# Optimization experiments

Hardware: AMD Instinct MI355X
Metric: run time of the kernel (lower is better)

Reference implementation:

```python
import jax, jax.numpy as jnp
import numpy as np

N_NODES = 50000
N_EDGES = 800000
D = 128
HEADS = 4
HEAD_DIM = D // HEADS
N_LAYERS = 3
NEG_SLOPE = 0.2


def setup_inputs() -> dict:
    key = jax.random.key(0)
    ks = jax.random.split(key, 10)
    x = jax.random.normal(ks[0], (N_NODES, D), dtype=jnp.float32)
    edge_index = jax.random.randint(ks[1], (2, N_EDGES), 0, N_NODES, dtype=jnp.int32)
    s = 1.0 / np.sqrt(D)
    gcn_w = jax.random.normal(ks[2], (N_LAYERS, D, D), dtype=jnp.float32) * s
    gcn_b = jnp.zeros((N_LAYERS, D), dtype=jnp.float32)
    gat_w = jax.random.normal(ks[3], (N_LAYERS, D, D), dtype=jnp.float32) * s
    gat_att_src = jax.random.normal(ks[4], (N_LAYERS, HEADS, HEAD_DIM), dtype=jnp.float32) * s
    gat_att_dst = jax.random.normal(ks[5], (N_LAYERS, HEADS, HEAD_DIM), dtype=jnp.float32) * s
    gat_b = jnp.zeros((N_LAYERS, D), dtype=jnp.float32)
    ln_g = jnp.ones((N_LAYERS, D), dtype=jnp.float32)
    ln_b = jnp.zeros((N_LAYERS, D), dtype=jnp.float32)
    return {"x": x, "edge_index": edge_index, "gcn_w": gcn_w, "gcn_b": gcn_b,
            "gat_w": gat_w, "gat_att_src": gat_att_src, "gat_att_dst": gat_att_dst,
            "gat_b": gat_b, "ln_g": ln_g, "ln_b": ln_b}


def _gcn(x, src, dst, n, w, b):
    # PyG GCNConv: self-loops (already in src/dst), symmetric normalization
    xw = x @ w                                             # [N, D]
    deg = jax.ops.segment_sum(jnp.ones_like(dst, dtype=xw.dtype), dst, num_segments=n)
    dinv = jax.lax.rsqrt(deg)                              # deg >= 1 due to self-loops
    norm = dinv[src] * dinv[dst]                           # [E]
    out = jax.ops.segment_sum(xw[src] * norm[:, None], dst, num_segments=n)
    return out + b


def _gat(x, src, dst, n, w, att_src, att_dst, b):
    # PyG GATConv, concat heads, self-loops already in src/dst
    xw = (x @ w).reshape(n, HEADS, HEAD_DIM)               # [N, H, Dh]
    a_src = (xw * att_src).sum(-1)                         # [N, H]
    a_dst = (xw * att_dst).sum(-1)                         # [N, H]
    e = jax.nn.leaky_relu(a_src[src] + a_dst[dst], NEG_SLOPE)  # [E, H]
    m = jax.ops.segment_max(e, dst, num_segments=n)        # [N, H]
    ee = jnp.exp(e - m[dst])
    z = jax.ops.segment_sum(ee, dst, num_segments=n)       # [N, H]
    alpha = ee / z[dst]                                    # [E, H]
    out = jax.ops.segment_sum(xw[src] * alpha[:, :, None], dst, num_segments=n)
    return out.reshape(n, HEADS * HEAD_DIM) + b


def _layernorm(x, g, b, eps=1e-5):
    mu = x.mean(-1, keepdims=True)
    var = ((x - mu) ** 2).mean(-1, keepdims=True)
    return (x - mu) * jax.lax.rsqrt(var + eps) * g + b


def reference(x, edge_index, gcn_w, gcn_b, gat_w, gat_att_src, gat_att_dst, gat_b, ln_g, ln_b):
    n = x.shape[0]
    loops = jnp.arange(n, dtype=edge_index.dtype)
    src = jnp.concatenate([edge_index[0], loops])
    dst = jnp.concatenate([edge_index[1], loops])
    h = x
    for i in range(N_LAYERS):
        h_gcn = _gcn(h, src, dst, n, gcn_w[i], gcn_b[i])
        h_att = _gat(h_gcn, src, dst, n, gat_w[i], gat_att_src[i], gat_att_dst[i], gat_b[i])
        h = _layernorm(h_att + h_gcn, ln_g[i], ln_b[i])
        h = jax.nn.relu(h)  # dropout is identity in eval mode
    return h
```

## Files before the change

### kernel.cpp

```cpp
#include <hip/hip_runtime.h>

#define NN 50000
#define NE 800000
#define NOUT (NN * 128)
#define PF_TOTAL 100608

typedef unsigned int u32;
typedef unsigned short u16;

typedef __attribute__((ext_vector_type(4))) float f32x4;
typedef __attribute__((ext_vector_type(8))) short bf16x8;

__device__ __forceinline__ float bf2f(u16 u) { return __uint_as_float(((u32)u) << 16); }
__device__ __forceinline__ u32 f2bf_u(float f) {
  u32 u = __float_as_uint(f);
  u += 0x7FFFu + ((u >> 16) & 1u);
  return u >> 16;
}
__device__ __forceinline__ u32 pk2(float a, float b) {
  return f2bf_u(a) | (f2bf_u(b) << 16);
}
__device__ __forceinline__ float lo_f(u32 v) { return __uint_as_float(v << 16); }
__device__ __forceinline__ float hi_f(u32 v) { return __uint_as_float(v & 0xFFFF0000u); }
__device__ __forceinline__ float h2f(u16 h) {
  u32 sg = ((u32)h >> 15) & 1u, e = ((u32)h >> 10) & 0x1Fu, mm = (u32)h & 0x3FFu;
  u32 o;
  if (e == 0u) o = sg << 31;
  else if (e == 31u) o = (sg << 31) | 0x7F800000u | (mm << 13);
  else o = (sg << 31) | ((e + 112u) << 23) | (mm << 13);
  return __uint_as_float(o);
}
__device__ __forceinline__ float lrelu(float x) { return x > 0.f ? x : 0.2f * x; }
__device__ __forceinline__ u32 umin32(u32 a, u32 b) { return a < b ? a : b; }

__device__ __forceinline__ float cvt_one(const void* p, int j, u32 fmode) {
  if (fmode == 1u) return ((const float*)p)[j];
  if (fmode == 2u) return h2f(((const u16*)p)[j]);
  return bf2f(((const u16*)p)[j]);
}

__global__ __launch_bounds__(256) void MultiScaleGNN_54769422958784_kernel(
    float* out, float val, int n) {
  int i = blockIdx.x * 256 + threadIdx.x;
  if (i < n) out[i] = val;
}

__global__ __launch_bounds__(64) void detect_kernel(const u32* lng, const int* ei,
                                                    u32* flag) {
  if (threadIdx.x == 0) {
    u32 v0 = lng[0], v1 = lng[1];
    u32 fm;
    if (v0 == 0x3F803F80u && v1 == 0x3F803F80u) fm = 0u;
    else if (v0 == 0x3F800000u && v1 == 0x3F800000u) fm = 1u;
    else if (v0 == 0x3C003C00u && v1 == 0x3C003C00u) fm = 2u;
    else fm = 1u;
    flag[0] = fm;
    flag[1] = ((ei[1] | ei[3] | ei[5] | ei[7]) == 0) ? 1u : 0u;
  }
}

__global__ __launch_bounds__(256) void cvt_x_kernel(const void* in, u32* outh, int n64,
                                                    const u32* flag) {
  u32 fm = flag[0];
  int i = blockIdx.x * 256 + threadIdx.x;
  if (i >= n64) return;
  int node = i >> 6, w = i & 63;
  float a = cvt_one(in, node * 128 + w * 2, fm);
  float b = cvt_one(in, node * 128 + w * 2 + 1, fm);
  outh[i] = pk2(a, b);
}

__global__ __launch_bounds__(256) void cvt_params_kernel(const void* g0, const void* g1,
                                                         const void* g2, const void* g3,
                                                         const void* g4, const void* g5,
                                                         const void* g6, const void* g7,
                                                         float* out, const u32* flag) {
  u32 fm = flag[0];
  int i = blockIdx.x * 256 + threadIdx.x;
  if (i >= PF_TOTAL) return;
  int offs[9] = {0, 49152, 49536, 98688, 99072, 99456, 99840, 100224, 100608};
  const void* ptrs[8] = {g0, g1, g2, g3, g4, g5, g6, g7};
  int r = 0;
  while (i >= offs[r + 1]) r++;
  out[i] = cvt_one(ptrs[r], i - offs[r], fm);
}

__global__ __launch_bounds__(256) void cvt_wt_kernel(const float* __restrict__ pf,
                                                     u32* __restrict__ wt) {
  int i = blockIdx.x * 256 + threadIdx.x;
  if (i >= 49152) return;
  int mat = i >> 13;
  int rem = i & 8191;
  int kk = rem >> 7;
  int n = rem & 127;
  const float* W = pf + (mat < 3 ? (size_t)mat * 16384 : 49536 + (size_t)(mat - 3) * 16384);
  float a = W[(2 * kk) * 128 + n];
  float b = W[(2 * kk + 1) * 128 + n];
  wt[(size_t)mat * 8192 + n * 64 + kk] = pk2(a, b);
}

__global__ __launch_bounds__(256) void zero1_kernel(u32* a, int n) {
  int i = blockIdx.x * 256 + threadIdx.x;
  if (i < n) a[i] = 0u;
}

__global__ __launch_bounds__(256) void rank_kernel(const int* ei, u32* cnt, u32* rank,
                                                   int e, int n, const u32* flag) {
  int i = blockIdx.x * blockDim.x + threadIdx.x;
  if (i >= e) return;
  int d = flag[1] ? ei[2 * e + 2 * i] : ei[e + i];
  u32 r = 0u;
  if ((u32)d < (u32)n) r = atomicAdd(&cnt[d], 1u);
  rank[i] = r;
}

__device__ __forceinline__ u32 wave_incl_scan(u32 v, int lane) {
#pragma unroll
  for (int off = 1; off < 64; off <<= 1) {
    u32 t = (u32)__shfl_up((int)v, off);
    if (lane >= off) v += t;
  }
  return v;
}

__global__ __launch_bounds__(256) void scan_sum_kernel(const u32* counts, u32* bsums,
                                                       int n) {
  __shared__ u32 ws[4];
  int i = blockIdx.x * 256 + threadIdx.x;
  int lane = threadIdx.x & 63, wid = threadIdx.x >> 6;
  u32 c = (i < n) ? counts[i] : 0u;
#pragma unroll
  for (int off = 32; off; off >>= 1) c += (u32)__shfl_xor((int)c, off);
  if (lane == 0) ws[wid] = c;
  __syncthreads();
  if (threadIdx.x == 0) bsums[blockIdx.x] = ws[0] + ws[1] + ws[2] + ws[3];
}

__global__ __launch_bounds__(256) void scan_bsums_kernel(u32* bsums, u32* rowptr, int nb,
                                                         int n) {
  __shared__ u32 ws[4];
  int tid = threadIdx.x, lane = tid & 63, wid = tid >> 6;
  u32 v = (tid < nb) ? bsums[tid] : 0u;
  u32 incl = wave_incl_scan(v, lane);
  if (lane == 63) ws[wid] = incl;
  __syncthreads();
  u32 wo = 0u;
  for (int w = 0; w < wid; w++) wo += ws[w];
  u32 excl = incl - v + wo;
  if (tid < nb) bsums[tid] = excl;
  if (tid == 0) rowptr[n] = ws[0] + ws[1] + ws[2] + ws[3];
}

__global__ __launch_bounds__(256) void scan_write_kernel(const u32* counts,
                                                         const u32* bsums, u32* rowptr,
                                                         float* dinv, int n) {
  __shared__ u32 ws[4];
  int b = blockIdx.x;
  int i = b * 256 + threadIdx.x;
  int lane = threadIdx.x & 63, wid = threadIdx.x >> 6;
  u32 c = (i < n) ? counts[i] : 0u;
  u32 incl = wave_incl_scan(c, lane);
  if (lane == 63) ws[wid] = incl;
  __syncthreads();
  u32 wo = bsums[b];
  for (int w = 0; w < wid; w++) wo += ws[w];
  u32 excl = incl - c + wo;
  if (i < n) {
    rowptr[i] = excl;
    dinv[i] = rsqrtf((float)(c + 1u));
  }
}

__global__ __launch_bounds__(256) void place_kernel(const int* ei, const u32* rowptr,
                                                    const u32* rank, int* col, int e,
                                                    int n, const u32* flag) {
  int i = blockIdx.x * blockDim.x + threadIdx.x;
  if (i >= e) return;
  u32 em = flag[1];
  int s = em ? ei[2 * i] : ei[i];
  int d = em ? ei[2 * e + 2 * i] : ei[e + i];
  if ((u32)d >= (u32)n) return;
  u32 p = rowptr[d] + rank[i];
  if (p < (u32)e) col[p] = ((u32)s < (u32)n) ? s : 0;
}

__global__ __launch_bounds__(256) void gemm_mfma_kernel(
    const u32* __restrict__ Ah, const u32* __restrict__ WTh, u32* __restrict__ Oh,
    const float* __restrict__ dinv, const float* __restrict__ att_s,
    const float* __restrict__ att_d, float* __restrict__ asrc,
    float* __restrict__ adst, int M) {
  int tid = threadIdx.x;
  int wave = tid >> 6, lane = tid & 63;
  int p = lane & 15, g = lane >> 4;
  int r0 = blockIdx.x * 128 + wave * 32;
  int ra = r0 + p, rb = r0 + 16 + p;
  int rac = min(ra, M - 1), rbc = min(rb, M - 1);

  const u32* apA = Ah + (size_t)rac * 64 + g * 4;
  const u32* apB = Ah + (size_t)rbc * 64 + g * 4;
  uint4 bA[4], bB[4];
#pragma unroll
  for (int k0 = 0; k0 < 4; k0++) {
    bA[k0] = *(const uint4*)(apA + k0 * 16);
    bB[k0] = *(const uint4*)(apB + k0 * 16);
  }

  f32x4 acc0[8], acc1[8];
#pragma unroll
  for (int t = 0; t < 8; t++) {
    acc0[t] = (f32x4)0.f;
    acc1[t] = (f32x4)0.f;
  }

  const u32* wp = WTh + p * 64 + g * 4;
#pragma unroll
  for (int k0 = 0; k0 < 4; k0++) {
    bf16x8 fa = __builtin_bit_cast(bf16x8, bA[k0]);
    bf16x8 fb = __builtin_bit_cast(bf16x8, bB[k0]);
#pragma unroll
    for (int t = 0; t < 8; t++) {
      uint4 af = *(const uint4*)(wp + t * 1024 + k0 * 16);
      bf16x8 aw = __builtin_bit_cast(bf16x8, af);
      acc0[t] = __builtin_amdgcn_mfma_f32_16x16x32_bf16(aw, fa, acc0[t], 0, 0, 0);
      acc1[t] = __builtin_amdgcn_mfma_f32_16x16x32_bf16(aw, fb, acc1[t], 0, 0, 0);
    }
  }

#pragma unroll
  for (int i = 0; i < 2; i++) {
    int r = r0 + i * 16 + p;
    if (r < M) {
      float sc = dinv ? dinv[r] : 1.0f;
      u32* orow = Oh + (size_t)r * 64;
      float hs[4] = {0.f, 0.f, 0.f, 0.f};
      float hd[4] = {0.f, 0.f, 0.f, 0.f};
#pragma unroll
      for (int t = 0; t < 8; t++) {
        f32x4 v = (i == 0) ? acc0[t] : acc1[t];
        float v0 = v[0] * sc, v1 = v[1] * sc, v2 = v[2] * sc, v3 = v[3] * sc;
        *(uint2*)(orow + t * 8 + g * 2) = make_uint2(pk2(v0, v1), pk2(v2, v3));
        if (att_s) {
          float4 wsv = *(const float4*)(att_s + t * 16 + g * 4);
          float4 wdv = *(const float4*)(att_d + t * 16 + g * 4);
          int h = t >> 1;
          hs[h] += v0 * wsv.x + v1 * wsv.y + v2 * wsv.z + v3 * wsv.w;
          hd[h] += v0 * wdv.x + v1 * wdv.y + v2 * wdv.z + v3 * wdv.w;
        }
      }
      if (att_s) {
#pragma unroll
        for (int h = 0; h < 4; h++) {
          hs[h] += __shfl_xor(hs[h], 16);
          hs[h] += __shfl_xor(hs[h], 32);
          hd[h] += __shfl_xor(hd[h], 16);
          hd[h] += __shfl_xor(hd[h], 32);
        }
        if (g == 0) {
          *(float4*)(asrc + (size_t)r * 4) = make_float4(hs[0], hs[1], hs[2], hs[3]);
          *(float4*)(adst + (size_t)r * 4) = make_float4(hd[0], hd[1], hd[2], hd[3]);
        }
      }
    }
  }
}

__global__ __launch_bounds__(256) void gcn_agg_kernel(const u32* __restrict__ xh,
                                                      const int* col, const u32* rowptr,
                                                      const float* dinv, const float* bias,
                                                      u32* __restrict__ outh, int n) {
  __shared__ int lds_s[8][32];
  int g = threadIdx.x >> 5;
  int l = threadIdx.x & 31;
  int d = blockIdx.x * 8 + g;
  if (d >= n) return;
  u32 start = umin32(rowptr[d], (u32)NE), end = umin32(rowptr[d + 1], (u32)NE);
  float4 acc = make_float4(0.f, 0.f, 0.f, 0.f);
  for (u32 base = start; base < end; base += 32) {
    u32 i = base + l;
    int cnt = (int)umin32(32u, end - base);
    if (i < end) lds_s[g][l] = col[i];
#pragma unroll 4
    for (int j = 0; j < cnt; j++) {
      int s = lds_s[g][j];
      uint2 v = *(const uint2*)(xh + (size_t)s * 64 + l * 2);
      acc.x += lo_f(v.x);
      acc.y += hi_f(v.x);
      acc.z += lo_f(v.y);
      acc.w += hi_f(v.y);
    }
  }
  int c0 = l * 4;
  uint2 sv = *(const uint2*)(xh + (size_t)d * 64 + l * 2);
  float dd = dinv[d];
  float o0 = dd * (acc.x + lo_f(sv.x)) + bias[c0];
  float o1 = dd * (acc.y + hi_f(sv.x)) + bias[c0 + 1];
  float o2 = dd * (acc.z + lo_f(sv.y)) + bias[c0 + 2];
  float o3 = dd * (acc.w + hi_f(sv.y)) + bias[c0 + 3];
  *(uint2*)(outh + (size_t)d * 64 + l * 2) = make_uint2(pk2(o0, o1), pk2(o2, o3));
}

__global__ __launch_bounds__(256) void gat_agg_kernel(
    const u32* __restrict__ xh, const float* a_src4, const float* a_dst4, const int* col,
    const u32* rowptr, const u32* __restrict__ hgcnh, const float* gat_b,
    const float* ln_g, const float* ln_b, u32* __restrict__ outh,
    float* __restrict__ outf, int n) {
  __shared__ u32 lds_s[8][32];
  __shared__ float lds_ee[8][32][4];
  int g = threadIdx.x >> 5;
  int l = threadIdx.x & 31;
  int head4 = l >> 3;
  int d = blockIdx.x * 8 + g;
  if (d >= n) return;
  u32 start = umin32(rowptr[d], (u32)NE), end = umin32(rowptr[d + 1], (u32)NE);
  float4 ad = *(const float4*)(a_dst4 + (size_t)d * 4);
  float4 asl = *(const float4*)(a_src4 + (size_t)d * 4);
  float4 es;
  es.x = lrelu(asl.x + ad.x);
  es.y = lrelu(asl.y + ad.y);
  es.z = lrelu(asl.z + ad.z);
  es.w = lrelu(asl.w + ad.w);
  float4 m = es;
  float4 zp = make_float4(0.f, 0.f, 0.f, 0.f);
  float4 acc = make_float4(0.f, 0.f, 0.f, 0.f);
  for (u32 base = start; base < end; base += 32) {
    u32 i = base + l;
    int cnt = (int)umin32(32u, end - base);
    bool act = i < end;
    float4 lg = make_float4(-1e30f, -1e30f, -1e30f, -1e30f);
    int s = 0;
    if (act) {
      s = col[i];
      float4 a = *(const float4*)(a_src4 + (size_t)s * 4);
      lg.x = lrelu(a.x + ad.x);
      lg.y = lrelu(a.y + ad.y);
      lg.z = lrelu(a.z + ad.z);
      lg.w = lrelu(a.w + ad.w);
    }
    float4 cm = lg;
#pragma unroll
    for (int off = 16; off; off >>= 1) {
      cm.x = fmaxf(cm.x, __shfl_xor(cm.x, off));
      cm.y = fmaxf(cm.y, __shfl_xor(cm.y, off));
      cm.z = fmaxf(cm.z, __shfl_xor(cm.z, off));
      cm.w = fmaxf(cm.w, __shfl_xor(cm.w, off));
    }
    float4 mn;
    mn.x = fmaxf(m.x, cm.x);
    mn.y = fmaxf(m.y, cm.y);
    mn.z = fmaxf(m.z, cm.z);
    mn.w = fmaxf(m.w, cm.w);
    float4 f;
    f.x = __expf(m.x - mn.x);
    f.y = __expf(m.y - mn.y);
    f.z = __expf(m.z - mn.z);
    f.w = __expf(m.w - mn.w);
    m = mn;
    zp.x *= f.x;
    zp.y *= f.y;
    zp.z *= f.z;
    zp.w *= f.w;
    float fsel = (head4 == 0) ? f.x : (head4 == 1) ? f.y : (head4 == 2) ? f.z : f.w;
    acc.x *= fsel;
    acc.y *= fsel;
    acc.z *= fsel;
    acc.w *= fsel;
    if (act) {
      float ex = __expf(lg.x - m.x);
      float ey = __expf(lg.y - m.y);
      float ez = __expf(lg.z - m.z);
      float ew = __expf(lg.w - m.w);
      zp.x += ex;
      zp.y += ey;
      zp.z += ez;
      zp.w += ew;
      lds_s[g][l] = (u32)s;
      *(float4*)&lds_ee[g][l][0] = make_float4(ex, ey, ez, ew);
    }
#pragma unroll 4
    for (int j = 0; j < cnt; j++) {
      u32 sg = lds_s[g][j];
      float w = lds_ee[g][j][head4];
      uint2 v = *(const uint2*)(xh + (size_t)sg * 64 + l * 2);
      acc.x = fmaf(w, lo_f(v.x), acc.x);
      acc.y = fmaf(w, hi_f(v.x), acc.y);
      acc.z = fmaf(w, lo_f(v.y), acc.z);
      acc.w = fmaf(w, hi_f(v.y), acc.w);
    }
  }
  float4 ees;
  ees.x = __expf(es.x - m.x);
  ees.y = __expf(es.y - m.y);
  ees.z = __expf(es.z - m.z);
  ees.w = __expf(es.w - m.w);
#pragma unroll
  for (int off = 16; off; off >>= 1) {
    zp.x += __shfl_xor(zp.x, off);
    zp.y += __shfl_xor(zp.y, off);
    zp.z += __shfl_xor(zp.z, off);
    zp.w += __shfl_xor(zp.w, off);
  }
  zp.x += ees.x;
  zp.y += ees.y;
  zp.z += ees.z;
  zp.w += ees.w;
  float wsel = (head4 == 0) ? ees.x : (head4 == 1) ? ees.y : (head4 == 2) ? ees.z : ees.w;
  float zsel = (head4 == 0) ? zp.x : (head4 == 1) ? zp.y : (head4 == 2) ? zp.z : zp.w;
  int c0 = l * 4;
  uint2 sv = *(const uint2*)(xh + (size_t)d * 64 + l * 2);
  acc.x = fmaf(wsel, lo_f(sv.x), acc.x);
  acc.y = fmaf(wsel, hi_f(sv.x), acc.y);
  acc.z = fmaf(wsel, lo_f(sv.y), acc.z);
  acc.w = fmaf(wsel, hi_f(sv.y), acc.w);
  float rz = 1.0f / zsel;
  uint2 hgv = *(const uint2*)(hgcnh + (size_t)d * 64 + l * 2);
  float t0 = acc.x * rz + gat_b[c0] + lo_f(hgv.x);
  float t1 = acc.y * rz + gat_b[c0 + 1] + hi_f(hgv.x);
  float t2 = acc.z * rz + gat_b[c0 + 2] + lo_f(hgv.y);
  float t3 = acc.w * rz + gat_b[c0 + 3] + hi_f(hgv.y);
  float ssum = t0 + t1 + t2 + t3;
#pragma unroll
  for (int off = 16; off; off >>= 1) ssum += __shfl_xor(ssum, off);
  float mu = ssum * (1.0f / 128.0f);
  float d0 = t0 - mu, d1 = t1 - mu, d2 = t2 - mu, d3 = t3 - mu;
  float vv = d0 * d0 + d1 * d1 + d2 * d2 + d3 * d3;
#pragma unroll
  for (int off = 16; off; off >>= 1) vv += __shfl_xor(vv, off);
  float rstd = rsqrtf(vv * (1.0f / 128.0f) + 1e-5f);
  float o0 = fmaxf(fmaf(d0 * rstd, ln_g[c0], ln_b[c0]), 0.f);
  float o1 = fmaxf(fmaf(d1 * rstd, ln_g[c0 + 1], ln_b[c0 + 1]), 0.f);
  float o2 = fmaxf(fmaf(d2 * rstd, ln_g[c0 + 2], ln_b[c0 + 2]), 0.f);
  float o3 = fmaxf(fmaf(d3 * rstd, ln_g[c0 + 3], ln_b[c0 + 3]), 0.f);
  if (outf) {
    *(float4*)(outf + (size_t)d * 128 + c0) = make_float4(o0, o1, o2, o3);
  } else {
    *(uint2*)(outh + (size_t)d * 64 + l * 2) = make_uint2(pk2(o0, o1), pk2(o2, o3));
  }
}

extern "C" void kernel_launch(void* const* d_in, const int* in_sizes, int n_in,
                              void* d_out, int out_size, void* d_ws, size_t ws_size,
                              hipStream_t stream) {
  const int N = NN, E = NE;
  (void)in_sizes;
  (void)n_in;
  (void)out_size;
  (void)ws_size;

  char* ws = (char*)d_ws;
  size_t off = 0;
  u32* xwh = (u32*)(ws + off);      off += (size_t)N * 64 * 4;
  u32* hbufh = (u32*)(ws + off);    off += (size_t)N * 64 * 4;
  u32* hgcnh = (u32*)(ws + off);    off += (size_t)N * 64 * 4;
  float* asrc = (float*)(ws + off); off += (size_t)N * 4 * 4;
  float* adst = (float*)(ws + off); off += (size_t)N * 4 * 4;
  float* dinv = (float*)(ws + off); off += (size_t)N * 4;
  u32* counts = (u32*)(ws + off);   off += (size_t)N * 4;
  u32* rowptr = (u32*)(ws + off);   off += (size_t)(N + 1) * 4 + 252;
  u32* rank = (u32*)(ws + off);     off += (size_t)E * 4;
  int* col = (int*)(ws + off);      off += (size_t)E * 4;
  float* pf = (float*)(ws + off);   off += (size_t)PF_TOTAL * 4;
  u32* wt = (u32*)(ws + off);       off += (size_t)49152 * 4;
  u32* bsums = (u32*)(ws + off);    off += 256 * 4;
  u32* flag = (u32*)(ws + off);     off += 256;

  const int* edge_index = (const int*)d_in[1];
  detect_kernel<<<1, 64, 0, stream>>>((const u32*)d_in[8], edge_index, flag);
  cvt_params_kernel<<<(PF_TOTAL + 255) / 256, 256, 0, stream>>>(
      d_in[2], d_in[3], d_in[4], d_in[5], d_in[6], d_in[7], d_in[8], d_in[9], pf, flag);
  cvt_wt_kernel<<<(49152 + 255) / 256, 256, 0, stream>>>(pf, wt);
  cvt_x_kernel<<<(N * 64 + 255) / 256, 256, 0, stream>>>(d_in[0], hbufh, N * 64, flag);
  zero1_kernel<<<(N + 255) / 256, 256, 0, stream>>>(counts, N);
  rank_kernel<<<(E + 255) / 256, 256, 0, stream>>>(edge_index, counts, rank, E, N, flag);
  {
    int nb = (N + 255) / 256;
    scan_sum_kernel<<<nb, 256, 0, stream>>>(counts, bsums, N);
    scan_bsums_kernel<<<1, 256, 0, stream>>>(bsums, rowptr, nb, N);
    scan_write_kernel<<<nb, 256, 0, stream>>>(counts, bsums, rowptr, dinv, N);
  }
  place_kernel<<<(E + 255) / 256, 256, 0, stream>>>(edge_index, rowptr, rank, col, E, N,
                                                    flag);

  const float* att_s = pf + 98688;
  const float* att_d = pf + 99072;
  const float* gcn_b = pf + 49152;
  const float* gat_b = pf + 99456;
  const float* ln_g = pf + 99840;
  const float* ln_b = pf + 100224;

  int gblocks = (N + 127) / 128;
  int ablocks = (N + 7) / 8;
  for (int l = 0; l < 3; l++) {
    gemm_mfma_kernel<<<gblocks, 256, 0, stream>>>(
        hbufh, wt + (size_t)l * 8192, xwh, dinv, (const float*)0, (const float*)0,
        (float*)0, (float*)0, N);
    gcn_agg_kernel<<<ablocks, 256, 0, stream>>>(xwh, col, rowptr, dinv, gcn_b + l * 128,
                                                hgcnh, N);
    gemm_mfma_kernel<<<gblocks, 256, 0, stream>>>(
        hgcnh, wt + (size_t)(3 + l) * 8192, xwh, (const float*)0, att_s + l * 128,
        att_d + l * 128, asrc, adst, N);
    gat_agg_kernel<<<ablocks, 256, 0, stream>>>(
        xwh, asrc, adst, col, rowptr, hgcnh, gat_b + l * 128, ln_g + l * 128,
        ln_b + l * 128, hbufh, (l < 2) ? (float*)0 : (float*)d_out, N);
  }
}
```

Before: 476.3 us.

## Bucket CSR neighbours by source-index chunk to improve gather locality

Edges are counted and placed per (destination, source-chunk) bucket, using eight chunks over the node range. Within each destination row the neighbour list is therefore roughly grouped by source index, so the gathers in the aggregation kernels touch more nearby memory. The scan is widened to cover eight times as many counters, and degree normalisation moves into a separate kernel that reads the bucketed rowptr. Preprocessing gets more work, and any locality gain is small because the average degree is only about 16 per row.

```diff
diff --git a/kernel.cpp b/kernel.cpp
--- a/kernel.cpp
+++ b/kernel.cpp
@@ -4,6 +4,9 @@
 #define NE 800000
 #define NOUT (NN * 128)
 #define PF_TOTAL 100608
+#define NCHUNK 8
+#define CHUNKSZ 6250
+#define NC4 (NN * NCHUNK)
 
 typedef unsigned int u32;
 typedef unsigned short u16;
@@ -108,9 +111,12 @@
                                                    int e, int n, const u32* flag) {
   int i = blockIdx.x * blockDim.x + threadIdx.x;
   if (i >= e) return;
-  int d = flag[1] ? ei[2 * e + 2 * i] : ei[e + i];
+  u32 em = flag[1];
+  int s = em ? ei[2 * i] : ei[i];
+  int d = em ? ei[2 * e + 2 * i] : ei[e + i];
+  int sp = ((u32)s < (u32)n) ? s : 0;
   u32 r = 0u;
-  if ((u32)d < (u32)n) r = atomicAdd(&cnt[d], 1u);
+  if ((u32)d < (u32)n) r = atomicAdd(&cnt[d * NCHUNK + sp / CHUNKSZ], 1u);
   rank[i] = r;
 }
 
@@ -126,19 +132,21 @@
 __global__ __launch_bounds__(256) void scan_sum_kernel(const u32* counts, u32* bsums,
                                                        int n) {
   __shared__ u32 ws[4];
-  int i = blockIdx.x * 256 + threadIdx.x;
-  int lane = threadIdx.x & 63, wid = threadIdx.x >> 6;
-  u32 c = (i < n) ? counts[i] : 0u;
-#pragma unroll
-  for (int off = 32; off; off >>= 1) c += (u32)__shfl_xor((int)c, off);
-  if (lane == 0) ws[wid] = c;
+  int tid = threadIdx.x, lane = tid & 63, wid = tid >> 6;
+  int i0 = blockIdx.x * 1024 + tid * 4;
+  u32 t = 0u;
+#pragma unroll
+  for (int k = 0; k < 4; k++) t += (i0 + k < n) ? counts[i0 + k] : 0u;
+#pragma unroll
+  for (int off = 32; off; off >>= 1) t += (u32)__shfl_xor((int)t, off);
+  if (lane == 0) ws[wid] = t;
   __syncthreads();
-  if (threadIdx.x == 0) bsums[blockIdx.x] = ws[0] + ws[1] + ws[2] + ws[3];
-}
-
-__global__ __launch_bounds__(256) void scan_bsums_kernel(u32* bsums, u32* rowptr, int nb,
+  if (tid == 0) bsums[blockIdx.x] = ws[0] + ws[1] + ws[2] + ws[3];
+}
+
+__global__ __launch_bounds__(512) void scan_bsums_kernel(u32* bsums, u32* rowptr, int nb,
                                                          int n) {
-  __shared__ u32 ws[4];
+  __shared__ u32 ws[8];
   int tid = threadIdx.x, lane = tid & 63, wid = tid >> 6;
   u32 v = (tid < nb) ? bsums[tid] : 0u;
   u32 incl = wave_incl_scan(v, lane);
@@ -148,30 +156,49 @@
   for (int w = 0; w < wid; w++) wo += ws[w];
   u32 excl = incl - v + wo;
   if (tid < nb) bsums[tid] = excl;
-  if (tid == 0) rowptr[n] = ws[0] + ws[1] + ws[2] + ws[3];
+  if (tid == 0) {
+    u32 tot = 0u;
+    for (int w = 0; w < 8; w++) tot += ws[w];
+    rowptr[n] = tot;
+  }
 }
 
 __global__ __launch_bounds__(256) void scan_write_kernel(const u32* counts,
                                                          const u32* bsums, u32* rowptr,
-                                                         float* dinv, int n) {
+                                                         int n) {
   __shared__ u32 ws[4];
+  int tid = threadIdx.x, lane = tid & 63, wid = tid >> 6;
   int b = blockIdx.x;
-  int i = b * 256 + threadIdx.x;
-  int lane = threadIdx.x & 63, wid = threadIdx.x >> 6;
-  u32 c = (i < n) ? counts[i] : 0u;
-  u32 incl = wave_incl_scan(c, lane);
+  int i0 = b * 1024 + tid * 4;
+  u32 c0 = (i0 + 0 < n) ? counts[i0 + 0] : 0u;
+  u32 c1 = (i0 + 1 < n) ? counts[i0 + 1] : 0u;
+  u32 c2 = (i0 + 2 < n) ? counts[i0 + 2] : 0u;
+  u32 c3 = (i0 + 3 < n) ? counts[i0 + 3] : 0u;
+  u32 ts = c0 + c1 + c2 + c3;
+  u32 incl = wave_incl_scan(ts, lane);
   if (lane == 63) ws[wid] = incl;
   __syncthreads();
   u32 wo = bsums[b];
   for (int w = 0; w < wid; w++) wo += ws[w];
-  u32 excl = incl - c + wo;
-  if (i < n) {
-    rowptr[i] = excl;
-    dinv[i] = rsqrtf((float)(c + 1u));
-  }
-}
-
-__global__ __launch_bounds__(256) void place_kernel(const int* ei, const u32* rowptr,
+  u32 excl = incl - ts + wo;
+  if (i0 + 0 < n) rowptr[i0 + 0] = excl;
+  excl += c0;
+  if (i0 + 1 < n) rowptr[i0 + 1] = excl;
+  excl += c1;
+  if (i0 + 2 < n) rowptr[i0 + 2] = excl;
+  excl += c2;
+  if (i0 + 3 < n) rowptr[i0 + 3] = excl;
+}
+
+__global__ __launch_bounds__(256) void dinv_kernel(const u32* __restrict__ rowptr4,
+                                                   float* __restrict__ dinv, int nn) {
+  int i = blockIdx.x * 256 + threadIdx.x;
+  if (i < nn)
+    dinv[i] = rsqrtf((float)(rowptr4[(size_t)i * NCHUNK + NCHUNK] -
+                             rowptr4[(size_t)i * NCHUNK] + 1u));
+}
+
+__global__ __launch_bounds__(256) void place_kernel(const int* ei, const u32* rowptr4,
                                                     const u32* rank, int* col, int e,
                                                     int n, const u32* flag) {
   int i = blockIdx.x * blockDim.x + threadIdx.x;
@@ -180,8 +207,9 @@
   int s = em ? ei[2 * i] : ei[i];
   int d = em ? ei[2 * e + 2 * i] : ei[e + i];
   if ((u32)d >= (u32)n) return;
-  u32 p = rowptr[d] + rank[i];
-  if (p < (u32)e) col[p] = ((u32)s < (u32)n) ? s : 0;
+  int sp = ((u32)s < (u32)n) ? s : 0;
+  u32 p = rowptr4[(size_t)d * NCHUNK + sp / CHUNKSZ] + rank[i];
+  if (p < (u32)e) col[p] = sp;
 }
 
 __global__ __launch_bounds__(256) void gemm_mfma_kernel(
@@ -265,7 +293,7 @@
 }
 
 __global__ __launch_bounds__(256) void gcn_agg_kernel(const u32* __restrict__ xh,
-                                                      const int* col, const u32* rowptr,
+                                                      const int* col, const u32* rowptr4,
                                                       const float* dinv, const float* bias,
                                                       u32* __restrict__ outh, int n) {
   __shared__ int lds_s[8][32];
@@ -273,7 +301,8 @@
   int l = threadIdx.x & 31;
   int d = blockIdx.x * 8 + g;
   if (d >= n) return;
-  u32 start = umin32(rowptr[d], (u32)NE), end = umin32(rowptr[d + 1], (u32)NE);
+  u32 start = umin32(rowptr4[(size_t)d * NCHUNK], (u32)NE);
+  u32 end = umin32(rowptr4[(size_t)d * NCHUNK + NCHUNK], (u32)NE);
   float4 acc = make_float4(0.f, 0.f, 0.f, 0.f);
   for (u32 base = start; base < end; base += 32) {
     u32 i = base + l;
@@ -301,7 +330,7 @@
 
 __global__ __launch_bounds__(256) void gat_agg_kernel(
     const u32* __restrict__ xh, const float* a_src4, const float* a_dst4, const int* col,
-    const u32* rowptr, const u32* __restrict__ hgcnh, const float* gat_b,
+    const u32* rowptr4, const u32* __restrict__ hgcnh, const float* gat_b,
     const float* ln_g, const float* ln_b, u32* __restrict__ outh,
     float* __restrict__ outf, int n) {
   __shared__ u32 lds_s[8][32];
@@ -311,7 +340,8 @@
   int head4 = l >> 3;
   int d = blockIdx.x * 8 + g;
   if (d >= n) return;
-  u32 start = umin32(rowptr[d], (u32)NE), end = umin32(rowptr[d + 1], (u32)NE);
+  u32 start = umin32(rowptr4[(size_t)d * NCHUNK], (u32)NE);
+  u32 end = umin32(rowptr4[(size_t)d * NCHUNK + NCHUNK], (u32)NE);
   float4 ad = *(const float4*)(a_dst4 + (size_t)d * 4);
   float4 asl = *(const float4*)(a_src4 + (size_t)d * 4);
   float4 es;
@@ -454,13 +484,13 @@
   float* asrc = (float*)(ws + off); off += (size_t)N * 4 * 4;
   float* adst = (float*)(ws + off); off += (size_t)N * 4 * 4;
   float* dinv = (float*)(ws + off); off += (size_t)N * 4;
-  u32* counts = (u32*)(ws + off);   off += (size_t)N * 4;
-  u32* rowptr = (u32*)(ws + off);   off += (size_t)(N + 1) * 4 + 252;
+  u32* counts4 = (u32*)(ws + off);  off += (size_t)NC4 * 4;
+  u32* rowptr4 = (u32*)(ws + off);  off += (size_t)(NC4 + 1) * 4 + 252;
   u32* rank = (u32*)(ws + off);     off += (size_t)E * 4;
   int* col = (int*)(ws + off);      off += (size_t)E * 4;
   float* pf = (float*)(ws + off);   off += (size_t)PF_TOTAL * 4;
   u32* wt = (u32*)(ws + off);       off += (size_t)49152 * 4;
-  u32* bsums = (u32*)(ws + off);    off += 256 * 4;
+  u32* bsums = (u32*)(ws + off);    off += 512 * 4;
   u32* flag = (u32*)(ws + off);     off += 256;
 
   const int* edge_index = (const int*)d_in[1];
@@ -469,15 +499,16 @@
       d_in[2], d_in[3], d_in[4], d_in[5], d_in[6], d_in[7], d_in[8], d_in[9], pf, flag);
   cvt_wt_kernel<<<(49152 + 255) / 256, 256, 0, stream>>>(pf, wt);
   cvt_x_kernel<<<(N * 64 + 255) / 256, 256, 0, stream>>>(d_in[0], hbufh, N * 64, flag);
-  zero1_kernel<<<(N + 255) / 256, 256, 0, stream>>>(counts, N);
-  rank_kernel<<<(E + 255) / 256, 256, 0, stream>>>(edge_index, counts, rank, E, N, flag);
+  zero1_kernel<<<(NC4 + 255) / 256, 256, 0, stream>>>(counts4, NC4);
+  rank_kernel<<<(E + 255) / 256, 256, 0, stream>>>(edge_index, counts4, rank, E, N, flag);
   {
-    int nb = (N + 255) / 256;
-    scan_sum_kernel<<<nb, 256, 0, stream>>>(counts, bsums, N);
-    scan_bsums_kernel<<<1, 256, 0, stream>>>(bsums, rowptr, nb, N);
-    scan_write_kernel<<<nb, 256, 0, stream>>>(counts, bsums, rowptr, dinv, N);
-  }
-  place_kernel<<<(E + 255) / 256, 256, 0, stream>>>(edge_index, rowptr, rank, col, E, N,
+    int nb = (NC4 + 1023) / 1024;
+    scan_sum_kernel<<<nb, 256, 0, stream>>>(counts4, bsums, NC4);
+    scan_bsums_kernel<<<1, 512, 0, stream>>>(bsums, rowptr4, nb, NC4);
+    scan_write_kernel<<<nb, 256, 0, stream>>>(counts4, bsums, rowptr4, NC4);
+  }
+  dinv_kernel<<<(N + 255) / 256, 256, 0, stream>>>(rowptr4, dinv, N);
+  place_kernel<<<(E + 255) / 256, 256, 0, stream>>>(edge_index, rowptr4, rank, col, E, N,
                                                     flag);
 
   const float* att_s = pf + 98688;
@@ -493,13 +524,13 @@
     gemm_mfma_kernel<<<gblocks, 256, 0, stream>>>(
         hbufh, wt + (size_t)l * 8192, xwh, dinv, (const float*)0, (const float*)0,
         (float*)0, (float*)0, N);
-    gcn_agg_kernel<<<ablocks, 256, 0, stream>>>(xwh, col, rowptr, dinv, gcn_b + l * 128,
+    gcn_agg_kernel<<<ablocks, 256, 0, stream>>>(xwh, col, rowptr4, dinv, gcn_b + l * 128,
                                                 hgcnh, N);
     gemm_mfma_kernel<<<gblocks, 256, 0, stream>>>(
         hgcnh, wt + (size_t)(3 + l) * 8192, xwh, (const float*)0, att_s + l * 128,
         att_d + l * 128, asrc, adst, N);
     gat_agg_kernel<<<ablocks, 256, 0, stream>>>(
-        xwh, asrc, adst, col, rowptr, hgcnh, gat_b + l * 128, ln_g + l * 128,
+        xwh, asrc, adst, col, rowptr4, hgcnh, gat_b + l * 128, ln_g + l * 128,
         ln_b + l * 128, hbufh, (l < 2) ? (float*)0 : (float*)d_out, N);
   }
 }
```

After: 479.0 us. No clear change (+0.6%).
